# Kernel optimization log

Hardware: AMD Instinct MI355X
Metric: run time of the kernel (lower is better)

The kernel has to match this reference:

```python
import jax, jax.numpy as jnp
import numpy as np

N_HEADS = 16


def setup_inputs() -> dict:
    key = jax.random.key(0)
    k1, k2, k3 = jax.random.split(key, 3)
    B, S, D = 2, 2048, 1024
    x = jax.random.normal(k1, (B, S, D), dtype=jnp.float32)
    w_qkv = jax.random.normal(k2, (D, 3 * D), dtype=jnp.float32) * 0.02
    b_qkv = jnp.zeros((3 * D,), dtype=jnp.float32)
    w_proj = jax.random.normal(k3, (D, D), dtype=jnp.float32) * 0.02
    b_proj = jnp.zeros((D,), dtype=jnp.float32)
    return {"x": x, "w_qkv": w_qkv, "b_qkv": b_qkv, "w_proj": w_proj, "b_proj": b_proj}


def reference(x, w_qkv, b_qkv, w_proj, b_proj):
    # Faithful to CausalAttention.flash_atttention: the blockwise online-softmax
    # loop computes exactly softmax(Q K^T / sqrt(hd) + causal_mask) V (no dropout).
    B, S, D = x.shape
    H = N_HEADS
    hd = D // H
    scale = 1.0 / jnp.sqrt(jnp.asarray(hd, dtype=x.dtype))

    qkv = x @ w_qkv + b_qkv                       # [B, S, 3D]
    q, k, v = jnp.split(qkv, 3, axis=-1)
    q = q.reshape(B, S, H, hd).transpose(0, 2, 1, 3)  # [B, H, S, hd]
    k = k.reshape(B, S, H, hd).transpose(0, 2, 1, 3)
    v = v.reshape(B, S, H, hd).transpose(0, 2, 1, 3)

    scores = jnp.einsum('bhqd,bhkd->bhqk', q, k) * scale  # [B, H, S, S]
    causal = jnp.tril(jnp.ones((S, S), dtype=bool))
    scores = jnp.where(causal, scores, -jnp.inf)
    attn = jax.nn.softmax(scores, axis=-1)
    out = jnp.einsum('bhqk,bhkd->bhqd', attn, v)  # [B, H, S, hd]
    out = out.transpose(0, 2, 1, 3).reshape(B, S, D)
    return out @ w_proj + b_proj
```

## Files before the change

### kernel.cpp

```cpp
#include <hip/hip_runtime.h>
#include <hip/hip_bf16.h>

typedef unsigned short u16;
typedef __attribute__((ext_vector_type(8))) short short8;
typedef __attribute__((ext_vector_type(4))) float floatx4;
typedef __attribute__((ext_vector_type(16))) float floatx16;

__device__ __forceinline__ u16 f2bf(float f) {
  union { float f; unsigned u; } v; v.f = f;
  unsigned r = v.u + 0x7fffu + ((v.u >> 16) & 1u);
  return (u16)(r >> 16);
}

__device__ __forceinline__ floatx4 mfma16(short8 a, short8 b, floatx4 c) {
  return __builtin_amdgcn_mfma_f32_16x16x32_bf16(a, b, c, 0, 0, 0);
}
__device__ __forceinline__ floatx16 mfma32(short8 a, short8 b, floatx16 c) {
  return __builtin_amdgcn_mfma_f32_32x32x16_bf16(a, b, c, 0, 0, 0);
}

#define AS1 __attribute__((address_space(1)))
#define AS3 __attribute__((address_space(3)))
__device__ __forceinline__ void gload_lds16(const u16* g, u16* l) {
  __builtin_amdgcn_global_load_lds((const AS1 void*)g, (AS3 void*)l, 16, 0, 0);
}

__device__ __forceinline__ unsigned pack2(float a, float b) {
  union { __hip_bfloat162 h; unsigned u; } x;
  x.h = __hip_bfloat162(__float2bfloat16(a), __float2bfloat16(b));
  return x.u;
}

__device__ __forceinline__ float fexp2(float x) {
#if __has_builtin(__builtin_amdgcn_exp2f)
  return __builtin_amdgcn_exp2f(x);
#else
  return exp2f(x);
#endif
}

#define WAIT_VM(N) asm volatile("s_waitcnt vmcnt(" #N ")" ::: "memory")
#define BARRIER()                      \
  do {                                 \
    __builtin_amdgcn_s_barrier();      \
    asm volatile("" ::: "memory");     \
  } while (0)

#define QSCALE 0.18033688f

__global__ void __launch_bounds__(256) f32_to_bf16_vec(
    const float* __restrict__ in, u16* __restrict__ out) {
  const int i = blockIdx.x * 256 + threadIdx.x;
  const float4* p = (const float4*)in + (size_t)i * 2;
  float4 a = p[0], b = p[1];
  short8 o;
  o[0] = (short)f2bf(a.x); o[1] = (short)f2bf(a.y);
  o[2] = (short)f2bf(a.z); o[3] = (short)f2bf(a.w);
  o[4] = (short)f2bf(b.x); o[5] = (short)f2bf(b.y);
  o[6] = (short)f2bf(b.z); o[7] = (short)f2bf(b.w);
  *(short8*)(out + (size_t)i * 8) = o;
}

__global__ void __launch_bounds__(256) transpose_f32_to_bf16(
    const float* __restrict__ in, u16* __restrict__ out, int R, int C) {
  __shared__ float tile[64][65];
  const int c0 = blockIdx.x * 64, r0 = blockIdx.y * 64;
  const int t = threadIdx.x;
  const int rr = t >> 2, cc = (t & 3) * 16;
  const float* src = in + (size_t)(r0 + rr) * C + (c0 + cc);
  float4 v0 = *(const float4*)(src);
  float4 v1 = *(const float4*)(src + 4);
  float4 v2 = *(const float4*)(src + 8);
  float4 v3 = *(const float4*)(src + 12);
  tile[rr][cc + 0] = v0.x;  tile[rr][cc + 1] = v0.y;
  tile[rr][cc + 2] = v0.z;  tile[rr][cc + 3] = v0.w;
  tile[rr][cc + 4] = v1.x;  tile[rr][cc + 5] = v1.y;
  tile[rr][cc + 6] = v1.z;  tile[rr][cc + 7] = v1.w;
  tile[rr][cc + 8] = v2.x;  tile[rr][cc + 9] = v2.y;
  tile[rr][cc + 10] = v2.z; tile[rr][cc + 11] = v2.w;
  tile[rr][cc + 12] = v3.x; tile[rr][cc + 13] = v3.y;
  tile[rr][cc + 14] = v3.z; tile[rr][cc + 15] = v3.w;
  __syncthreads();
  short8 w0, w1;
#pragma unroll
  for (int i = 0; i < 8; ++i) {
    w0[i] = (short)f2bf(tile[cc + i][rr]);
    w1[i] = (short)f2bf(tile[cc + 8 + i][rr]);
  }
  u16* dst = out + (size_t)(c0 + rr) * R + (r0 + cc);
  *(short8*)dst = w0;
  *(short8*)(dst + 8) = w1;
}

template <int EPI>
__global__ void __launch_bounds__(256, 2) gemm_bt(
    const u16* __restrict__ A, const u16* __restrict__ Bt,
    const float* __restrict__ bias, u16* __restrict__ O0,
    u16* __restrict__ O1, u16* __restrict__ O2, float* __restrict__ Of,
    int M, int N, int K) {
  __shared__ u16 As[2][8192];
  __shared__ u16 Bs[2][8192];
  const int t = threadIdx.x, w = t >> 6, l = t & 63;
  const int lo = l & 15, g = l >> 4;
  const int wr = w >> 1, wc = w & 1;
  const int m0 = blockIdx.y * 128, n0 = blockIdx.x * 128;
  const int srow = l >> 3;
  const int schunk = (l & 7) ^ srow;
  const u16* ApS = A + (size_t)(m0 + w * 32 + srow) * K + schunk * 8;
  const u16* BpS = Bt + (size_t)(n0 + w * 32 + srow) * K + schunk * 8;

  floatx4 acc[4][4] = {};
  const int NT = K >> 6;

#define STAGE_G(buf, kt_)                                                    \
  do {                                                                       \
    const size_t k0_ = (size_t)(kt_) * 64;                                   \
    _Pragma("unroll") for (int i = 0; i < 4; ++i)                            \
        gload_lds16(ApS + (size_t)i * 8 * K + k0_,                           \
                    &As[buf][(w * 4 + i) * 512]);                            \
    _Pragma("unroll") for (int i = 0; i < 4; ++i)                            \
        gload_lds16(BpS + (size_t)i * 8 * K + k0_,                           \
                    &Bs[buf][(w * 4 + i) * 512]);                            \
  } while (0)

#define COMPUTE_G(cur)                                                       \
  do {                                                                       \
    short8 af[2][4], bff[2][4];                                              \
    _Pragma("unroll") for (int kk = 0; kk < 2; ++kk)                         \
        _Pragma("unroll") for (int m = 0; m < 4; ++m) {                      \
      const int row = wr * 64 + m * 16 + lo;                                 \
      const int sl = (kk * 4 + g) ^ (lo & 7);                                \
      af[kk][m] = *(const short8*)(&As[cur][row * 64 + sl * 8]);             \
    }                                                                        \
    _Pragma("unroll") for (int kk = 0; kk < 2; ++kk)                         \
        _Pragma("unroll") for (int n = 0; n < 4; ++n) {                      \
      const int row = wc * 64 + n * 16 + lo;                                 \
      const int sl = (kk * 4 + g) ^ (lo & 7);                                \
      bff[kk][n] = *(const short8*)(&Bs[cur][row * 64 + sl * 8]);            \
    }                                                                        \
    __builtin_amdgcn_s_setprio(1);                                           \
    _Pragma("unroll") for (int kk = 0; kk < 2; ++kk)                         \
        _Pragma("unroll") for (int m = 0; m < 4; ++m)                        \
            _Pragma("unroll") for (int n = 0; n < 4; ++n) acc[m][n] =        \
                mfma16(af[kk][m], bff[kk][n], acc[m][n]);                    \
    __builtin_amdgcn_s_setprio(0);                                           \
  } while (0)

  STAGE_G(0, 0);
  int cur = 0;
  for (int kt = 0; kt < NT - 1; ++kt) {
    STAGE_G(cur ^ 1, kt + 1);
    WAIT_VM(8);
    BARRIER();
    COMPUTE_G(cur);
    BARRIER();
    cur ^= 1;
  }
  WAIT_VM(0);
  BARRIER();
  COMPUTE_G(cur);
#undef STAGE_G
#undef COMPUTE_G

#pragma unroll
  for (int m = 0; m < 4; ++m) {
    const int row_base = m0 + wr * 64 + m * 16 + g * 4;
#pragma unroll
    for (int n = 0; n < 4; ++n) {
      const int col = n0 + wc * 64 + n * 16 + lo;
      const float bv = bias[col];
#pragma unroll
      for (int j = 0; j < 4; ++j) {
        const int r = row_base + j;
        const float v = acc[m][n][j] + bv;
        if (EPI == 0) {
          const int b = r >> 11, s = r & 2047;
          int c = col;
          if (c < 1024) {
            const int hh = c >> 6, d = c & 63;
            O0[(((size_t)(b * 16 + hh)) * 2048 + s) * 64 + d] = f2bf(v * QSCALE);
          } else if (c < 2048) {
            c -= 1024;
            const int hh = c >> 6, d = c & 63;
            O1[(((size_t)(b * 16 + hh)) * 2048 + s) * 64 + d] = f2bf(v);
          } else {
            c -= 2048;
            const int hh = c >> 6, d = c & 63;
            O2[(((size_t)(b * 16 + hh)) * 64 + d) * 2048 + s] = f2bf(v);
          }
        } else {
          Of[(size_t)r * N + col] = v;
        }
      }
    }
  }
}

__global__ void __launch_bounds__(256, 2) attn_kernel(
    const u16* __restrict__ Q, const u16* __restrict__ K,
    const u16* __restrict__ Vt, u16* __restrict__ O) {
  const int S = 2048;
  __shared__ u16 smem[3][8192];
  const int t = threadIdx.x, w = t >> 6, l = t & 63;
  const int lo = l & 31, h = l >> 5;
  const int fid = blockIdx.x;
  const int half = fid >> 8, rdec = fid & 255;
  const int bh = half * 16 + (rdec >> 4);
  const int qb = half ? (15 - (rdec & 15)) : (rdec & 15);
  const int q0w = qb * 128 + w * 32;
  const int qmax = q0w + 31;
  const int qabs = q0w + lo;
  const u16* Qb = Q + (size_t)bh * S * 64;
  const u16* Kb = K + (size_t)bh * S * 64;
  const u16* Vb = Vt + (size_t)bh * 64 * S;

  short8 qf[4];
#pragma unroll
  for (int ks = 0; ks < 4; ++ks)
    qf[ks] = *(const short8*)(Qb + (size_t)(q0w + lo) * 64 + ks * 16 + h * 8);

  floatx16 o0 = {}, o1 = {};
  float m2 = -1e30f, ll = 0.f;

  auto STAGE = [&](int buf, int tile) {
    const int kv0 = tile * 64;
#pragma unroll
    for (int i = 0; i < 2; ++i) {
      const int idx = i * 256 + t;
      const int rw = idx >> 3;
      const int cg = (idx & 7) ^ (rw & 7);
      gload_lds16(Kb + (size_t)(kv0 + rw) * 64 + cg * 8,
                  &smem[buf][i * 2048 + w * 512]);
      gload_lds16(Vb + (size_t)rw * S + kv0 + cg * 8,
                  &smem[buf][4096 + i * 2048 + w * 512]);
    }
  };

  auto COMPUTE = [&](int cur, int kv0) {
    floatx16 st0 = {}, st1 = {};
    __builtin_amdgcn_s_setprio(1);
#pragma unroll
    for (int ks = 0; ks < 4; ++ks) {
      const int r0 = lo;
      short8 kf0 = *(const short8*)(
          &smem[cur][r0 * 64 + ((ks * 16 + h * 8) ^ ((r0 & 7) << 3))]);
      st0 = mfma32(kf0, qf[ks], st0);
      const int r1 = 32 + lo;
      short8 kf1 = *(const short8*)(
          &smem[cur][r1 * 64 + ((ks * 16 + h * 8) ^ ((r1 & 7) << 3))]);
      st1 = mfma32(kf1, qf[ks], st1);
    }
    __builtin_amdgcn_s_setprio(0);
    const bool diag = (kv0 + 63 > q0w);
    float p[2][16];
    float tmax = -1e30f;
#pragma unroll
    for (int rr = 0; rr < 16; ++rr) {
      float v0 = st0[rr];
      float v1 = st1[rr];
      if (diag) {
        const int kvr = kv0 + (rr & 3) + 8 * (rr >> 2) + 4 * h;
        if (kvr > qabs) v0 = -1e30f;
        if (kvr + 32 > qabs) v1 = -1e30f;
      }
      p[0][rr] = v0;
      p[1][rr] = v1;
      tmax = fmaxf(tmax, fmaxf(v0, v1));
    }
    tmax = fmaxf(tmax, __shfl_xor(tmax, 32));
    if (!__all(tmax <= m2 + 8.0f)) {
      const float mnew = fmaxf(m2, tmax);
      const float corr = fexp2(m2 - mnew);
      m2 = mnew;
      ll *= corr;
      o0 = o0 * corr;
      o1 = o1 * corr;
    }
    float tsum = 0.f;
#pragma unroll
    for (int nt = 0; nt < 2; ++nt)
#pragma unroll
      for (int rr = 0; rr < 16; ++rr) {
        const float e = fexp2(p[nt][rr] - m2);
        p[nt][rr] = e;
        tsum += e;
      }
    tsum += __shfl_xor(tsum, 32);
    ll += tsum;
    __builtin_amdgcn_s_setprio(1);
#pragma unroll
    for (int s = 0; s < 4; ++s) {
      const int ts = s >> 1, rb = (s & 1) * 8;
      const unsigned wA = pack2(p[ts][rb + 0], p[ts][rb + 1]);
      const unsigned wB = pack2(p[ts][rb + 2], p[ts][rb + 3]);
      const unsigned wC = pack2(p[ts][rb + 4], p[ts][rb + 5]);
      const unsigned wD = pack2(p[ts][rb + 6], p[ts][rb + 7]);
      union { unsigned u[4]; short8 s8; } bf;
#if __has_builtin(__builtin_amdgcn_permlane32_swap)
      auto r02 = __builtin_amdgcn_permlane32_swap((int)wA, (int)wC, false, false);
      auto r13 = __builtin_amdgcn_permlane32_swap((int)wB, (int)wD, false, false);
      bf.u[0] = (unsigned)r02[0];
      bf.u[1] = (unsigned)r13[0];
      bf.u[2] = (unsigned)r02[1];
      bf.u[3] = (unsigned)r13[1];
#else
      const unsigned sA = (unsigned)__shfl_xor((int)wA, 32);
      const unsigned sB = (unsigned)__shfl_xor((int)wB, 32);
      const unsigned sC = (unsigned)__shfl_xor((int)wC, 32);
      const unsigned sD = (unsigned)__shfl_xor((int)wD, 32);
      bf.u[0] = h ? sC : wA;
      bf.u[1] = h ? sD : wB;
      bf.u[2] = h ? wC : sA;
      bf.u[3] = h ? wD : sB;
#endif
      {
        const int r0 = lo;
        short8 vf = *(const short8*)(
            &smem[cur][4096 + r0 * 64 + ((s * 16 + h * 8) ^ ((r0 & 7) << 3))]);
        o0 = mfma32(vf, bf.s8, o0);
      }
      {
        const int r1 = 32 + lo;
        short8 vf = *(const short8*)(
            &smem[cur][4096 + r1 * 64 + ((s * 16 + h * 8) ^ ((r1 & 7) << 3))]);
        o1 = mfma32(vf, bf.s8, o1);
      }
    }
    __builtin_amdgcn_s_setprio(0);
  };

  const int T = 2 * (qb + 1);
  STAGE(0, 0);
  STAGE(1, 1);
  int cur = 0, stg = 2;
  for (int tt = 0; tt < T - 1; ++tt) {
    WAIT_VM(4);
    BARRIER();
    if (tt + 2 < T) STAGE(stg, tt + 2);
    const int kv0 = tt * 64;
    if (kv0 <= qmax) COMPUTE(cur, kv0);
    cur = (cur == 2) ? 0 : cur + 1;
    stg = (stg == 2) ? 0 : stg + 1;
  }
  WAIT_VM(0);
  BARRIER();
  {
    const int kv0 = (T - 1) * 64;
    if (kv0 <= qmax) COMPUTE(cur, kv0);
  }
  __syncthreads();

  const float rl = 1.0f / ll;
  u16* ep = &smem[0][w * 2048];
#pragma unroll
  for (int rr = 0; rr < 16; ++rr) {
    const int d0 = (rr & 3) + 8 * (rr >> 2) + 4 * h;
    ep[lo * 64 + (d0 ^ ((lo & 7) << 3))] = f2bf(o0[rr] * rl);
    const int d1 = d0 + 32;
    ep[lo * 64 + (d1 ^ ((lo & 7) << 3))] = f2bf(o1[rr] * rl);
  }
  const int hh = bh & 15, b = bh >> 4;
  u16* Ob = O + ((size_t)(b * 2048 + q0w)) * 1024 + hh * 64;
#pragma unroll
  for (int pp = 0; pp < 4; ++pp) {
    const int idx = pp * 64 + l;
    const int row = idx >> 3, c = idx & 7;
    short8 v = *(const short8*)(&ep[row * 64 + ((c * 8) ^ ((row & 7) << 3))]);
    *(short8*)(Ob + (size_t)row * 1024 + c * 8) = v;
  }
}

extern "C" void kernel_launch(void* const* d_in, const int* in_sizes, int n_in,
                              void* d_out, int out_size, void* d_ws,
                              size_t ws_size, hipStream_t stream) {
  const float* x = (const float*)d_in[0];
  const float* w_qkv = (const float*)d_in[1];
  const float* b_qkv = (const float*)d_in[2];
  const float* w_proj = (const float*)d_in[3];
  const float* b_proj = (const float*)d_in[4];
  float* out = (float*)d_out;

  char* ws = (char*)d_ws;
  u16* Xb = (u16*)(ws);
  u16* WqkvT = (u16*)(ws + 8388608);
  u16* WprojT = (u16*)(ws + 14680064);
  u16* Qw = (u16*)(ws + 16777216);
  u16* Kw = (u16*)(ws + 25165824);
  u16* Vtw = (u16*)(ws + 33554432);
  u16* AttnO = Xb;

  f32_to_bf16_vec<<<2048, 256, 0, stream>>>(x, Xb);
  transpose_f32_to_bf16<<<dim3(48, 16), 256, 0, stream>>>(w_qkv, WqkvT, 1024,
                                                          3072);
  transpose_f32_to_bf16<<<dim3(16, 16), 256, 0, stream>>>(w_proj, WprojT, 1024,
                                                          1024);
  gemm_bt<0><<<dim3(24, 32), 256, 0, stream>>>(Xb, WqkvT, b_qkv, Qw, Kw, Vtw,
                                               nullptr, 4096, 3072, 1024);
  attn_kernel<<<512, 256, 0, stream>>>(Qw, Kw, Vtw, AttnO);
  gemm_bt<1><<<dim3(8, 32), 256, 0, stream>>>(AttnO, WprojT, b_proj, nullptr,
                                              nullptr, nullptr, out, 4096, 1024,
                                              1024);
}
```

Before: 142.0 us.

## Split QKV GEMM into 256x128-tile 512-thread kernel, remap attention block order

The QKV projection gets its own kernel with 256x128 tiles, 512 threads, a single LDS buffer and a block order that walks M fastest. The output projection becomes a separate kernel that writes its results with nontemporal stores. The attention grid mapping now interleaves batch-heads across blocks and pairs short and long causal query blocks in a different order. The swizzle index switches from lo&7 to row&7, which is equivalent because the row offsets are multiples of 16. Dropping double buffering in the QKV GEMM removes load/compute overlap, in exchange for larger tiles and more waves per CU.

New measurement: 155.1 us. 9.2% more time.

```diff
diff --git a/kernel.cpp b/kernel.cpp
--- a/kernel.cpp
+++ b/kernel.cpp
@@ -92,12 +92,104 @@
   *(short8*)(dst + 8) = w1;
 }
 
-template <int EPI>
-__global__ void __launch_bounds__(256, 2) gemm_bt(
+__global__ void __launch_bounds__(512, 4) gemm_qkv(
     const u16* __restrict__ A, const u16* __restrict__ Bt,
     const float* __restrict__ bias, u16* __restrict__ O0,
-    u16* __restrict__ O1, u16* __restrict__ O2, float* __restrict__ Of,
-    int M, int N, int K) {
+    u16* __restrict__ O1, u16* __restrict__ O2) {
+  const int K = 1024;
+  __shared__ u16 As[256 * 64];
+  __shared__ u16 Bs[128 * 64];
+  const int t = threadIdx.x, w = t >> 6, l = t & 63;
+  const int lo = l & 15, g = l >> 4;
+  const int wr = w >> 1, wc = w & 1;
+  const int m0 = (blockIdx.x & 15) * 256;
+  const int n0 = (blockIdx.x >> 4) * 128;
+  const int srow = l >> 3;
+  const int schunk = (l & 7) ^ srow;
+  const u16* ApS = A + (size_t)(m0 + w * 32 + srow) * K + schunk * 8;
+  const u16* BpS = Bt + (size_t)(n0 + w * 16 + srow) * K + schunk * 8;
+
+  floatx4 acc[4][4] = {};
+
+#define STAGE_Q(kt_)                                                      \
+  do {                                                                    \
+    const size_t k0_ = (size_t)(kt_) * 64;                                \
+    _Pragma("unroll") for (int i = 0; i < 4; ++i)                         \
+        gload_lds16(ApS + (size_t)i * 8 * K + k0_,                        \
+                    &As[(w * 4 + i) * 512]);                              \
+    _Pragma("unroll") for (int i = 0; i < 2; ++i)                         \
+        gload_lds16(BpS + (size_t)i * 8 * K + k0_,                        \
+                    &Bs[(w * 2 + i) * 512]);                              \
+  } while (0)
+
+  STAGE_Q(0);
+  for (int kt = 0; kt < 16; ++kt) {
+    WAIT_VM(0);
+    BARRIER();
+    short8 af[2][4], bff[2][4];
+#pragma unroll
+    for (int kk = 0; kk < 2; ++kk)
+#pragma unroll
+      for (int m = 0; m < 4; ++m) {
+        const int row = wr * 64 + m * 16 + lo;
+        const int sl = (kk * 4 + g) ^ (row & 7);
+        af[kk][m] = *(const short8*)(&As[row * 64 + sl * 8]);
+      }
+#pragma unroll
+    for (int kk = 0; kk < 2; ++kk)
+#pragma unroll
+      for (int n = 0; n < 4; ++n) {
+        const int row = wc * 64 + n * 16 + lo;
+        const int sl = (kk * 4 + g) ^ (row & 7);
+        bff[kk][n] = *(const short8*)(&Bs[row * 64 + sl * 8]);
+      }
+    __builtin_amdgcn_s_setprio(1);
+#pragma unroll
+    for (int kk = 0; kk < 2; ++kk)
+#pragma unroll
+      for (int m = 0; m < 4; ++m)
+#pragma unroll
+        for (int n = 0; n < 4; ++n)
+          acc[m][n] = mfma16(af[kk][m], bff[kk][n], acc[m][n]);
+    __builtin_amdgcn_s_setprio(0);
+    BARRIER();
+    if (kt + 1 < 16) STAGE_Q(kt + 1);
+  }
+#undef STAGE_Q
+
+#pragma unroll
+  for (int m = 0; m < 4; ++m) {
+    const int row_base = m0 + wr * 64 + m * 16 + g * 4;
+#pragma unroll
+    for (int n = 0; n < 4; ++n) {
+      const int col = n0 + wc * 64 + n * 16 + lo;
+      const float bv = bias[col];
+#pragma unroll
+      for (int j = 0; j < 4; ++j) {
+        const int r = row_base + j;
+        const float v = acc[m][n][j] + bv;
+        const int b = r >> 11, s = r & 2047;
+        int c = col;
+        if (c < 1024) {
+          const int hh = c >> 6, d = c & 63;
+          O0[(((size_t)(b * 16 + hh)) * 2048 + s) * 64 + d] = f2bf(v * QSCALE);
+        } else if (c < 2048) {
+          c -= 1024;
+          const int hh = c >> 6, d = c & 63;
+          O1[(((size_t)(b * 16 + hh)) * 2048 + s) * 64 + d] = f2bf(v);
+        } else {
+          c -= 2048;
+          const int hh = c >> 6, d = c & 63;
+          O2[(((size_t)(b * 16 + hh)) * 64 + d) * 2048 + s] = f2bf(v);
+        }
+      }
+    }
+  }
+}
+
+__global__ void __launch_bounds__(256, 2) gemm_proj(
+    const u16* __restrict__ A, const u16* __restrict__ Bt,
+    const float* __restrict__ bias, float* __restrict__ Of, int N, int K) {
   __shared__ u16 As[2][8192];
   __shared__ u16 Bs[2][8192];
   const int t = threadIdx.x, w = t >> 6, l = t & 63;
@@ -112,7 +204,7 @@
   floatx4 acc[4][4] = {};
   const int NT = K >> 6;
 
-#define STAGE_G(buf, kt_)                                                    \
+#define STAGE_P(buf, kt_)                                                    \
   do {                                                                       \
     const size_t k0_ = (size_t)(kt_) * 64;                                   \
     _Pragma("unroll") for (int i = 0; i < 4; ++i)                            \
@@ -123,19 +215,19 @@
                     &Bs[buf][(w * 4 + i) * 512]);                            \
   } while (0)
 
-#define COMPUTE_G(cur)                                                       \
+#define COMPUTE_P(cur)                                                       \
   do {                                                                       \
     short8 af[2][4], bff[2][4];                                              \
     _Pragma("unroll") for (int kk = 0; kk < 2; ++kk)                         \
         _Pragma("unroll") for (int m = 0; m < 4; ++m) {                      \
       const int row = wr * 64 + m * 16 + lo;                                 \
-      const int sl = (kk * 4 + g) ^ (lo & 7);                                \
+      const int sl = (kk * 4 + g) ^ (row & 7);                               \
       af[kk][m] = *(const short8*)(&As[cur][row * 64 + sl * 8]);             \
     }                                                                        \
     _Pragma("unroll") for (int kk = 0; kk < 2; ++kk)                         \
         _Pragma("unroll") for (int n = 0; n < 4; ++n) {                      \
       const int row = wc * 64 + n * 16 + lo;                                 \
-      const int sl = (kk * 4 + g) ^ (lo & 7);                                \
+      const int sl = (kk * 4 + g) ^ (row & 7);                               \
       bff[kk][n] = *(const short8*)(&Bs[cur][row * 64 + sl * 8]);            \
     }                                                                        \
     __builtin_amdgcn_s_setprio(1);                                           \
@@ -146,21 +238,21 @@
     __builtin_amdgcn_s_setprio(0);                                           \
   } while (0)
 
-  STAGE_G(0, 0);
+  STAGE_P(0, 0);
   int cur = 0;
   for (int kt = 0; kt < NT - 1; ++kt) {
-    STAGE_G(cur ^ 1, kt + 1);
+    STAGE_P(cur ^ 1, kt + 1);
     WAIT_VM(8);
     BARRIER();
-    COMPUTE_G(cur);
+    COMPUTE_P(cur);
     BARRIER();
     cur ^= 1;
   }
   WAIT_VM(0);
   BARRIER();
-  COMPUTE_G(cur);
-#undef STAGE_G
-#undef COMPUTE_G
+  COMPUTE_P(cur);
+#undef STAGE_P
+#undef COMPUTE_P
 
 #pragma unroll
   for (int m = 0; m < 4; ++m) {
@@ -172,25 +264,8 @@
 #pragma unroll
       for (int j = 0; j < 4; ++j) {
         const int r = row_base + j;
-        const float v = acc[m][n][j] + bv;
-        if (EPI == 0) {
-          const int b = r >> 11, s = r & 2047;
-          int c = col;
-          if (c < 1024) {
-            const int hh = c >> 6, d = c & 63;
-            O0[(((size_t)(b * 16 + hh)) * 2048 + s) * 64 + d] = f2bf(v * QSCALE);
-          } else if (c < 2048) {
-            c -= 1024;
-            const int hh = c >> 6, d = c & 63;
-            O1[(((size_t)(b * 16 + hh)) * 2048 + s) * 64 + d] = f2bf(v);
-          } else {
-            c -= 2048;
-            const int hh = c >> 6, d = c & 63;
-            O2[(((size_t)(b * 16 + hh)) * 64 + d) * 2048 + s] = f2bf(v);
-          }
-        } else {
-          Of[(size_t)r * N + col] = v;
-        }
+        __builtin_nontemporal_store(acc[m][n][j] + bv,
+                                    &Of[(size_t)r * N + col]);
       }
     }
   }
@@ -203,10 +278,10 @@
   __shared__ u16 smem[3][8192];
   const int t = threadIdx.x, w = t >> 6, l = t & 63;
   const int lo = l & 31, h = l >> 5;
-  const int fid = blockIdx.x;
-  const int half = fid >> 8, rdec = fid & 255;
-  const int bh = half * 16 + (rdec >> 4);
-  const int qb = half ? (15 - (rdec & 15)) : (rdec & 15);
+  const int wg = blockIdx.x;
+  const int bh = (wg & 7) * 4 + ((wg >> 3) & 3);
+  const int qidx = wg >> 5;
+  const int qb = (qidx < 8) ? qidx : 23 - qidx;
   const int q0w = qb * 128 + w * 32;
   const int qmax = q0w + 31;
   const int qabs = q0w + lo;
@@ -394,10 +469,8 @@
                                                           3072);
   transpose_f32_to_bf16<<<dim3(16, 16), 256, 0, stream>>>(w_proj, WprojT, 1024,
                                                           1024);
-  gemm_bt<0><<<dim3(24, 32), 256, 0, stream>>>(Xb, WqkvT, b_qkv, Qw, Kw, Vtw,
-                                               nullptr, 4096, 3072, 1024);
+  gemm_qkv<<<384, 512, 0, stream>>>(Xb, WqkvT, b_qkv, Qw, Kw, Vtw);
   attn_kernel<<<512, 256, 0, stream>>>(Qw, Kw, Vtw, AttnO);
-  gemm_bt<1><<<dim3(8, 32), 256, 0, stream>>>(AttnO, WprojT, b_proj, nullptr,
-                                              nullptr, nullptr, out, 4096, 1024,
-                                              1024);
-}
+  gemm_proj<<<dim3(8, 32), 256, 0, stream>>>(AttnO, WprojT, b_proj, out, 1024,
+                                             1024);
+}
```
